# Performance work log

Hardware: AMD Instinct MI355X
Metric: run time of the kernel (lower is better)

Reference implementation:

```python
import jax, jax.numpy as jnp
import numpy as np

VOCAB = 50257
B, T, D = 32, 2048, 512


def setup_inputs() -> dict:
    key = jax.random.key(0)
    k1, k2, k3 = jax.random.split(key, 3)
    vector_sequence = jax.random.normal(k1, (B, T, D), dtype=jnp.float32)
    # lengths in [1, T] to match realistic sentence lengths (avoids 0/0 in y)
    sentence_length = jax.random.randint(k2, (B,), 1, T + 1, dtype=jnp.int32)
    word_sequence = jax.random.randint(k3, (B, T), 0, VOCAB, dtype=jnp.int32)
    # ParameterDict of scalars flattened to one vector, init = 1/num_of_vocab
    weights = jnp.ones((VOCAB,), dtype=jnp.float32) / VOCAB
    return {
        "vector_sequence": vector_sequence,
        "sentence_length": sentence_length,
        "word_sequence": word_sequence,
        "weights": weights,
    }


def reference(vector_sequence, sentence_length, word_sequence, weights):
    # mask out positions >= sentence_length (original zeroes them in place)
    mask = (jnp.arange(T)[None, :] < sentence_length[:, None]).astype(
        vector_sequence.dtype
    )  # [B, T]
    vs = vector_sequence * mask[:, :, None]  # [B, T, D]
    # y = sum_t vs / sum_t |vs|  (per batch, per dim)
    y = jnp.sum(vs, axis=1) / jnp.sum(jnp.abs(vs), axis=1)  # [B, D]
    # per-token scalar weight gather; padded positions are already zero in vs
    w = weights[word_sequence]  # [B, T]
    y_hat = jnp.sum(vs * w[:, :, None], axis=1)  # [B, D]
    return (y, y_hat)
```

## Files before the change

### kernel.cpp

```cpp
#include <hip/hip_runtime.h>

#define NB 32
#define NT 2048
#define ND 512
#define NDQ 128

__global__ __launch_bounds__(256) void vu_partial_kernel(
    const float* __restrict__ vs,
    const int* __restrict__ slen,
    const int* __restrict__ wseq,
    const float* __restrict__ weights,
    float4* __restrict__ ps,
    float4* __restrict__ pa,
    float4* __restrict__ pw,
    int NC)
{
    const int c   = blockIdx.x;
    const int b   = blockIdx.y;
    const int tid = threadIdx.x;
    const int dq  = tid & (NDQ - 1);
    const int tt  = tid >> 7;
    const int TC  = NT / NC;

    __shared__ float w_lds[NT];
    __shared__ float red[NDQ * 12];

    const int t0   = c * TC;
    const int len  = slen[b];
    const int tEnd = min(t0 + TC, len);

    for (int i = tid; i < TC; i += 256) {
        const int t = t0 + i;
        float w = 0.0f;
        if (t < tEnd) w = weights[wseq[b * NT + t]];
        w_lds[i] = w;
    }
    __syncthreads();

    float4 s  = make_float4(0.f, 0.f, 0.f, 0.f);
    float4 sa = make_float4(0.f, 0.f, 0.f, 0.f);
    float4 sw = make_float4(0.f, 0.f, 0.f, 0.f);

    const float4* vsq = (const float4*)vs;
    for (int t = t0 + tt; t < tEnd; t += 2) {
        const float4 v = vsq[((size_t)b * NT + t) * NDQ + dq];
        const float  w = w_lds[t - t0];
        s.x += v.x; s.y += v.y; s.z += v.z; s.w += v.w;
        sa.x += fabsf(v.x); sa.y += fabsf(v.y); sa.z += fabsf(v.z); sa.w += fabsf(v.w);
        sw.x += v.x * w; sw.y += v.y * w; sw.z += v.z * w; sw.w += v.w * w;
    }

    if (tt == 1) {
        float* r = &red[dq * 12];
        r[0] = s.x;  r[1] = s.y;  r[2]  = s.z;  r[3]  = s.w;
        r[4] = sa.x; r[5] = sa.y; r[6]  = sa.z; r[7]  = sa.w;
        r[8] = sw.x; r[9] = sw.y; r[10] = sw.z; r[11] = sw.w;
    }
    __syncthreads();
    if (tt == 0) {
        const float* r = &red[dq * 12];
        s.x += r[0];  s.y += r[1];  s.z += r[2];   s.w += r[3];
        sa.x += r[4]; sa.y += r[5]; sa.z += r[6];  sa.w += r[7];
        sw.x += r[8]; sw.y += r[9]; sw.z += r[10]; sw.w += r[11];
        const size_t o = ((size_t)b * NC + c) * NDQ + dq;
        ps[o] = s;
        pa[o] = sa;
        pw[o] = sw;
    }
}

__global__ __launch_bounds__(256) void vu_reduce_kernel(
    const float4* __restrict__ ps,
    const float4* __restrict__ pa,
    const float4* __restrict__ pw,
    float4* __restrict__ out,
    int NC)
{
    const int gid = blockIdx.x * 256 + threadIdx.x;
    if (gid >= NB * NDQ) return;
    const int b  = gid >> 7;
    const int dq = gid & (NDQ - 1);

    float4 s  = make_float4(0.f, 0.f, 0.f, 0.f);
    float4 sa = make_float4(0.f, 0.f, 0.f, 0.f);
    float4 sw = make_float4(0.f, 0.f, 0.f, 0.f);
    for (int c = 0; c < NC; ++c) {
        const size_t o = ((size_t)b * NC + c) * NDQ + dq;
        const float4 a = ps[o];
        const float4 x = pa[o];
        const float4 w = pw[o];
        s.x += a.x; s.y += a.y; s.z += a.z; s.w += a.w;
        sa.x += x.x; sa.y += x.y; sa.z += x.z; sa.w += x.w;
        sw.x += w.x; sw.y += w.y; sw.z += w.z; sw.w += w.w;
    }
    float4 y;
    y.x = s.x / sa.x; y.y = s.y / sa.y; y.z = s.z / sa.z; y.w = s.w / sa.w;
    out[(size_t)b * NDQ + dq] = y;
    out[(size_t)NB * NDQ + (size_t)b * NDQ + dq] = sw;
}

extern "C" void kernel_launch(void* const* d_in, const int* in_sizes, int n_in,
                              void* d_out, int out_size, void* d_ws, size_t ws_size,
                              hipStream_t stream) {
    const float* vs      = (const float*)d_in[0];
    const int*   slen    = (const int*)d_in[1];
    const int*   wseq    = (const int*)d_in[2];
    const float* weights = (const float*)d_in[3];
    float4*      out     = (float4*)d_out;

    int NC = 64;
    while (NC > 1) {
        size_t need = (size_t)NB * NC * ND * 3 * sizeof(float);
        if (need <= ws_size) break;
        NC >>= 1;
    }

    const size_t stride = (size_t)NB * NC * NDQ;
    float4* ps = (float4*)d_ws;
    float4* pa = ps + stride;
    float4* pw = pa + stride;

    dim3 g1(NC, NB);
    vu_partial_kernel<<<g1, 256, 0, stream>>>(vs, slen, wseq, weights, ps, pa, pw, NC);

    const int n2 = NB * NDQ;
    vu_reduce_kernel<<<(n2 + 255) / 256, 256, 0, stream>>>(ps, pa, pw, out, NC);
}
```

Before: 204.9 us.

## Use one thread per float4 column, drop LDS reduction, skip empty chunks

Each partial block now runs 128 threads, and each thread walks its whole time chunk alone with an unrolled loop. This removes the two-way split and the shared-memory reduction with its extra barrier. Blocks whose chunk lies entirely past the sentence length exit early, and the reduce kernel reads only the chunks that were written. NC is now fixed at 64 with no check against the workspace size, and halving the block size lowers the number of in-flight loads per CU.

```diff
diff --git a/kernel.cpp b/kernel.cpp
--- a/kernel.cpp
+++ b/kernel.cpp
@@ -4,36 +4,31 @@
 #define NT 2048
 #define ND 512
 #define NDQ 128
+#define NC 64
+#define TC (NT / NC)
 
-__global__ __launch_bounds__(256) void vu_partial_kernel(
+__global__ __launch_bounds__(128) void vu_partial_kernel(
     const float* __restrict__ vs,
     const int* __restrict__ slen,
     const int* __restrict__ wseq,
     const float* __restrict__ weights,
     float4* __restrict__ ps,
     float4* __restrict__ pa,
-    float4* __restrict__ pw,
-    int NC)
+    float4* __restrict__ pw)
 {
-    const int c   = blockIdx.x;
-    const int b   = blockIdx.y;
-    const int tid = threadIdx.x;
-    const int dq  = tid & (NDQ - 1);
-    const int tt  = tid >> 7;
-    const int TC  = NT / NC;
-
-    __shared__ float w_lds[NT];
-    __shared__ float red[NDQ * 12];
+    const int c  = blockIdx.x;
+    const int b  = blockIdx.y;
+    const int dq = threadIdx.x;
 
     const int t0   = c * TC;
     const int len  = slen[b];
     const int tEnd = min(t0 + TC, len);
+    if (t0 >= tEnd) return;
 
-    for (int i = tid; i < TC; i += 256) {
-        const int t = t0 + i;
-        float w = 0.0f;
-        if (t < tEnd) w = weights[wseq[b * NT + t]];
-        w_lds[i] = w;
+    __shared__ float w_lds[TC];
+    if (threadIdx.x < TC) {
+        const int t = t0 + threadIdx.x;
+        w_lds[threadIdx.x] = (t < tEnd) ? weights[wseq[b * NT + t]] : 0.0f;
     }
     __syncthreads();
 
@@ -42,49 +37,41 @@
     float4 sw = make_float4(0.f, 0.f, 0.f, 0.f);
 
     const float4* vsq = (const float4*)vs;
-    for (int t = t0 + tt; t < tEnd; t += 2) {
+    #pragma unroll 4
+    for (int t = t0; t < tEnd; ++t) {
         const float4 v = vsq[((size_t)b * NT + t) * NDQ + dq];
         const float  w = w_lds[t - t0];
         s.x += v.x; s.y += v.y; s.z += v.z; s.w += v.w;
         sa.x += fabsf(v.x); sa.y += fabsf(v.y); sa.z += fabsf(v.z); sa.w += fabsf(v.w);
-        sw.x += v.x * w; sw.y += v.y * w; sw.z += v.z * w; sw.w += v.w * w;
+        sw.x = fmaf(v.x, w, sw.x); sw.y = fmaf(v.y, w, sw.y);
+        sw.z = fmaf(v.z, w, sw.z); sw.w = fmaf(v.w, w, sw.w);
     }
 
-    if (tt == 1) {
-        float* r = &red[dq * 12];
-        r[0] = s.x;  r[1] = s.y;  r[2]  = s.z;  r[3]  = s.w;
-        r[4] = sa.x; r[5] = sa.y; r[6]  = sa.z; r[7]  = sa.w;
-        r[8] = sw.x; r[9] = sw.y; r[10] = sw.z; r[11] = sw.w;
-    }
-    __syncthreads();
-    if (tt == 0) {
-        const float* r = &red[dq * 12];
-        s.x += r[0];  s.y += r[1];  s.z += r[2];   s.w += r[3];
-        sa.x += r[4]; sa.y += r[5]; sa.z += r[6];  sa.w += r[7];
-        sw.x += r[8]; sw.y += r[9]; sw.z += r[10]; sw.w += r[11];
-        const size_t o = ((size_t)b * NC + c) * NDQ + dq;
-        ps[o] = s;
-        pa[o] = sa;
-        pw[o] = sw;
-    }
+    const size_t o = ((size_t)b * NC + c) * NDQ + dq;
+    ps[o] = s;
+    pa[o] = sa;
+    pw[o] = sw;
 }
 
 __global__ __launch_bounds__(256) void vu_reduce_kernel(
     const float4* __restrict__ ps,
     const float4* __restrict__ pa,
     const float4* __restrict__ pw,
-    float4* __restrict__ out,
-    int NC)
+    const int* __restrict__ slen,
+    float4* __restrict__ out)
 {
     const int gid = blockIdx.x * 256 + threadIdx.x;
     if (gid >= NB * NDQ) return;
     const int b  = gid >> 7;
     const int dq = gid & (NDQ - 1);
 
+    const int len  = slen[b];
+    const int cEnd = (len + TC - 1) / TC;
+
     float4 s  = make_float4(0.f, 0.f, 0.f, 0.f);
     float4 sa = make_float4(0.f, 0.f, 0.f, 0.f);
     float4 sw = make_float4(0.f, 0.f, 0.f, 0.f);
-    for (int c = 0; c < NC; ++c) {
+    for (int c = 0; c < cEnd; ++c) {
         const size_t o = ((size_t)b * NC + c) * NDQ + dq;
         const float4 a = ps[o];
         const float4 x = pa[o];
@@ -108,21 +95,14 @@
     const float* weights = (const float*)d_in[3];
     float4*      out     = (float4*)d_out;
 
-    int NC = 64;
-    while (NC > 1) {
-        size_t need = (size_t)NB * NC * ND * 3 * sizeof(float);
-        if (need <= ws_size) break;
-        NC >>= 1;
-    }
-
     const size_t stride = (size_t)NB * NC * NDQ;
     float4* ps = (float4*)d_ws;
     float4* pa = ps + stride;
     float4* pw = pa + stride;
 
     dim3 g1(NC, NB);
-    vu_partial_kernel<<<g1, 256, 0, stream>>>(vs, slen, wseq, weights, ps, pa, pw, NC);
+    vu_partial_kernel<<<g1, 128, 0, stream>>>(vs, slen, wseq, weights, ps, pa, pw);
 
     const int n2 = NB * NDQ;
-    vu_reduce_kernel<<<(n2 + 255) / 256, 256, 0, stream>>>(ps, pa, pw, out, NC);
+    vu_reduce_kernel<<<(n2 + 255) / 256, 256, 0, stream>>>(ps, pa, pw, slen, out);
 }
```

Result: no change. 204.5 us (-0.2%).
